# Kernel optimization log

Hardware: AMD Instinct MI355X
Metric: run time of the kernel (lower is better)

## Reference

```python
import jax, jax.numpy as jnp
import numpy as np

N = 262144          # batch (flattened batch*time)
D = 128             # internal_dim
OBS_DIMS = (100000, 50000)
ACT_DIMS = (1000, 1000)


def setup_inputs() -> dict:
    key = jax.random.key(0)
    ks = jax.random.split(key, 8)
    return {
        "obs0": jax.random.randint(ks[0], (N,), 0, OBS_DIMS[0], dtype=jnp.int32),
        "obs1": jax.random.randint(ks[1], (N,), 0, OBS_DIMS[1], dtype=jnp.int32),
        "act0": jax.random.randint(ks[2], (N,), 0, ACT_DIMS[0], dtype=jnp.int32),
        "act1": jax.random.randint(ks[3], (N,), 0, ACT_DIMS[1], dtype=jnp.int32),
        "w_state0": jax.random.normal(ks[4], (OBS_DIMS[0], D), dtype=jnp.float32) * 0.01,
        "w_state1": jax.random.normal(ks[5], (OBS_DIMS[1], D), dtype=jnp.float32) * 0.01,
        "w_act0": jax.random.normal(ks[6], (ACT_DIMS[0], D), dtype=jnp.float32) * 0.01,
        "w_act1": jax.random.normal(ks[7], (ACT_DIMS[1], D), dtype=jnp.float32) * 0.01,
        "bias": jnp.zeros((D,), dtype=jnp.float32),
    }


def reference(obs0, obs1, act0, act1, w_state0, w_state1, w_act0, w_act1, bias):
    # tf.one_hot(idx, V) @ W  ==  row-gather W[idx]; accumulate all fields + bias.
    out = (bias[None, :]
           + w_state0[obs0]    # [N, D]
           + w_state1[obs1]
           + w_act0[act0]
           + w_act1[act1])
    return out
```

## Files before the change

kernel.cpp:

```cpp
#include <hip/hip_runtime.h>


#define PE_N 262144
#define PE_D 128
#define ROWS_PER_BLOCK 16

typedef float v4f __attribute__((ext_vector_type(4)));

__global__ __launch_bounds__(256) void PolicyEncoder_79044578116211_kernel(
    const int* __restrict__ obs0, const int* __restrict__ obs1,
    const int* __restrict__ act0, const int* __restrict__ act1,
    const float* __restrict__ w_state0, const float* __restrict__ w_state1,
    const float* __restrict__ w_act0, const float* __restrict__ w_act1,
    const float* __restrict__ bias, float* __restrict__ out)
{
    const int t    = threadIdx.x;
    const int slot = t >> 5;
    const int lane = t & 31;

    const int rowA = blockIdx.x * ROWS_PER_BLOCK + slot;
    const int rowB = rowA + 8;

    const int iA0 = obs0[rowA], iB0 = obs0[rowB];
    const int iA1 = obs1[rowA], iB1 = obs1[rowB];
    const int aA0 = act0[rowA], aB0 = act0[rowB];
    const int aA1 = act1[rowA], aB1 = act1[rowB];

    const unsigned lofs = (unsigned)lane * 16u;

    v4f xb = *(const v4f*)((const char*)bias + lofs);

    v4f A0 = *(const v4f*)((const char*)w_state0 + (((unsigned)iA0) << 9) + lofs);
    v4f A1 = *(const v4f*)((const char*)w_state1 + (((unsigned)iA1) << 9) + lofs);
    v4f A2 = *(const v4f*)((const char*)w_act0   + (((unsigned)aA0) << 9) + lofs);
    v4f A3 = *(const v4f*)((const char*)w_act1   + (((unsigned)aA1) << 9) + lofs);
    v4f B0 = *(const v4f*)((const char*)w_state0 + (((unsigned)iB0) << 9) + lofs);
    v4f B1 = *(const v4f*)((const char*)w_state1 + (((unsigned)iB1) << 9) + lofs);
    v4f B2 = *(const v4f*)((const char*)w_act0   + (((unsigned)aB0) << 9) + lofs);
    v4f B3 = *(const v4f*)((const char*)w_act1   + (((unsigned)aB1) << 9) + lofs);

    __builtin_amdgcn_sched_barrier(0);

    v4f accA = (xb + A0) + (A1 + A2) + A3;
    v4f accB = (xb + B0) + (B1 + B2) + B3;

    v4f* outA = (v4f*)((char*)out + (size_t)rowA * (PE_D * 4) + lofs);
    v4f* outB = (v4f*)((char*)out + (size_t)rowB * (PE_D * 4) + lofs);
    __builtin_nontemporal_store(accA, outA);
    __builtin_nontemporal_store(accB, outB);
}

extern "C" void kernel_launch(void* const* d_in, const int* in_sizes, int n_in,
                              void* d_out, int out_size, void* d_ws, size_t ws_size,
                              hipStream_t stream) {
    const int*   obs0     = (const int*)  d_in[0];
    const int*   obs1     = (const int*)  d_in[1];
    const int*   act0     = (const int*)  d_in[2];
    const int*   act1     = (const int*)  d_in[3];
    const float* w_state0 = (const float*)d_in[4];
    const float* w_state1 = (const float*)d_in[5];
    const float* w_act0   = (const float*)d_in[6];
    const float* w_act1   = (const float*)d_in[7];
    const float* bias     = (const float*)d_in[8];
    float*       out      = (float*)d_out;

    const int grid = PE_N / ROWS_PER_BLOCK;
    PolicyEncoder_79044578116211_kernel<<<grid, 256, 0, stream>>>(
        obs0, obs1, act0, act1, w_state0, w_state1, w_act0, w_act1, bias, out);
}
```

Before: 237.5 us.

## Use persistent blocks with software-pipelined gathers across row iterations

Replaces the one-shot grid of 16384 blocks with 2048 blocks that each loop over 16 iterations of 8 rows. The loop double-buffers the index loads and row gathers, prefetching the next row's embeddings and the indices two iterations ahead while the current row is summed and stored. The aim is to cut block launch overhead and keep memory requests in flight. The cost is fewer loads in flight per thread (one row instead of two), and the sched_barrier on every iteration may keep the compiler from interleaving work.

```diff
diff --git a/kernel.cpp b/kernel.cpp
--- a/kernel.cpp
+++ b/kernel.cpp
@@ -3,11 +3,14 @@
 
 #define PE_N 262144
 #define PE_D 128
-#define ROWS_PER_BLOCK 16
+#define PE_BLOCKS 2048
+#define PE_THREADS 256
+#define ROWS_PER_ITER 8
+#define PE_ITERS (PE_N / (PE_BLOCKS * ROWS_PER_ITER))
 
 typedef float v4f __attribute__((ext_vector_type(4)));
 
-__global__ __launch_bounds__(256) void PolicyEncoder_79044578116211_kernel(
+__global__ __launch_bounds__(PE_THREADS) void PolicyEncoder_79044578116211_kernel(
     const int* __restrict__ obs0, const int* __restrict__ obs1,
     const int* __restrict__ act0, const int* __restrict__ act1,
     const float* __restrict__ w_state0, const float* __restrict__ w_state1,
@@ -17,37 +20,51 @@
     const int t    = threadIdx.x;
     const int slot = t >> 5;
     const int lane = t & 31;
-
-    const int rowA = blockIdx.x * ROWS_PER_BLOCK + slot;
-    const int rowB = rowA + 8;
-
-    const int iA0 = obs0[rowA], iB0 = obs0[rowB];
-    const int iA1 = obs1[rowA], iB1 = obs1[rowB];
-    const int aA0 = act0[rowA], aB0 = act0[rowB];
-    const int aA1 = act1[rowA], aB1 = act1[rowB];
-
     const unsigned lofs = (unsigned)lane * 16u;
 
-    v4f xb = *(const v4f*)((const char*)bias + lofs);
+    const int base = blockIdx.x * (ROWS_PER_ITER * PE_ITERS) + slot;
 
-    v4f A0 = *(const v4f*)((const char*)w_state0 + (((unsigned)iA0) << 9) + lofs);
-    v4f A1 = *(const v4f*)((const char*)w_state1 + (((unsigned)iA1) << 9) + lofs);
-    v4f A2 = *(const v4f*)((const char*)w_act0   + (((unsigned)aA0) << 9) + lofs);
-    v4f A3 = *(const v4f*)((const char*)w_act1   + (((unsigned)aA1) << 9) + lofs);
-    v4f B0 = *(const v4f*)((const char*)w_state0 + (((unsigned)iB0) << 9) + lofs);
-    v4f B1 = *(const v4f*)((const char*)w_state1 + (((unsigned)iB1) << 9) + lofs);
-    v4f B2 = *(const v4f*)((const char*)w_act0   + (((unsigned)aB0) << 9) + lofs);
-    v4f B3 = *(const v4f*)((const char*)w_act1   + (((unsigned)aB1) << 9) + lofs);
+    const v4f xb = *(const v4f*)((const char*)bias + lofs);
 
-    __builtin_amdgcn_sched_barrier(0);
+    int i0[2], i1[2], a0[2], a1[2];
+    v4f g0[2], g1[2], g2[2], g3[2];
 
-    v4f accA = (xb + A0) + (A1 + A2) + A3;
-    v4f accB = (xb + B0) + (B1 + B2) + B3;
+    {
+        const int r0 = base;
+        i0[0] = obs0[r0]; i1[0] = obs1[r0]; a0[0] = act0[r0]; a1[0] = act1[r0];
+        const int r1 = base + ROWS_PER_ITER;
+        i0[1] = obs0[r1]; i1[1] = obs1[r1]; a0[1] = act0[r1]; a1[1] = act1[r1];
+        g0[0] = *(const v4f*)((const char*)w_state0 + (((unsigned)i0[0]) << 9) + lofs);
+        g1[0] = *(const v4f*)((const char*)w_state1 + (((unsigned)i1[0]) << 9) + lofs);
+        g2[0] = *(const v4f*)((const char*)w_act0   + (((unsigned)a0[0]) << 9) + lofs);
+        g3[0] = *(const v4f*)((const char*)w_act1   + (((unsigned)a1[0]) << 9) + lofs);
+    }
 
-    v4f* outA = (v4f*)((char*)out + (size_t)rowA * (PE_D * 4) + lofs);
-    v4f* outB = (v4f*)((char*)out + (size_t)rowB * (PE_D * 4) + lofs);
-    __builtin_nontemporal_store(accA, outA);
-    __builtin_nontemporal_store(accB, outB);
+    #pragma unroll
+    for (int i = 0; i < PE_ITERS; ++i) {
+        const int cur = i & 1;
+        const int nxt = (i + 1) & 1;
+
+        if (i + 1 < PE_ITERS) {
+            g0[nxt] = *(const v4f*)((const char*)w_state0 + (((unsigned)i0[nxt]) << 9) + lofs);
+            g1[nxt] = *(const v4f*)((const char*)w_state1 + (((unsigned)i1[nxt]) << 9) + lofs);
+            g2[nxt] = *(const v4f*)((const char*)w_act0   + (((unsigned)a0[nxt]) << 9) + lofs);
+            g3[nxt] = *(const v4f*)((const char*)w_act1   + (((unsigned)a1[nxt]) << 9) + lofs);
+        }
+
+        if (i + 2 < PE_ITERS) {
+            const int r2 = base + (i + 2) * ROWS_PER_ITER;
+            i0[cur] = obs0[r2]; i1[cur] = obs1[r2];
+            a0[cur] = act0[r2]; a1[cur] = act1[r2];
+        }
+
+        __builtin_amdgcn_sched_barrier(0);
+
+        v4f acc = ((xb + g0[cur]) + (g1[cur] + g2[cur])) + g3[cur];
+
+        v4f* o = (v4f*)((char*)out + (size_t)(base + i * ROWS_PER_ITER) * (PE_D * 4) + lofs);
+        __builtin_nontemporal_store(acc, o);
+    }
 }
 
 extern "C" void kernel_launch(void* const* d_in, const int* in_sizes, int n_in,
@@ -64,7 +81,6 @@
     const float* bias     = (const float*)d_in[8];
     float*       out      = (float*)d_out;
 
-    const int grid = PE_N / ROWS_PER_BLOCK;
-    PolicyEncoder_79044578116211_kernel<<<grid, 256, 0, stream>>>(
+    PolicyEncoder_79044578116211_kernel<<<PE_BLOCKS, PE_THREADS, 0, stream>>>(
         obs0, obs1, act0, act1, w_state0, w_state1, w_act0, w_act1, bias, out);
 }
```

After: 240.9 us. No clear change (+1.4%).
